# Performance work log

Hardware: AMD Instinct MI355X
Metric: run time of the kernel (lower is better)

The kernel has to match this reference:

```python
import jax, jax.numpy as jnp
import numpy as np

B, S, D, H, DFF = 2, 2048, 768, 12, 3072
DH = D // H
EPS = 1e-5


def _ln(x, g, b):
    m = jnp.mean(x, axis=-1, keepdims=True)
    v = jnp.mean((x - m) ** 2, axis=-1, keepdims=True)
    return (x - m) * jax.lax.rsqrt(v + EPS) * g + b


def setup_inputs() -> dict:
    key = jax.random.key(0)
    ks = jax.random.split(key, 13)
    sd = 1.0 / np.sqrt(D)
    sf = 1.0 / np.sqrt(DFF)
    return {
        "x": jax.random.normal(ks[0], (B, S, D), jnp.float32),
        "Wq": jax.random.uniform(ks[1], (D, D), jnp.float32, -sd, sd),
        "bq": jnp.zeros((D,), jnp.float32),
        "Wk": jax.random.uniform(ks[2], (D, D), jnp.float32, -sd, sd),
        "bk": jnp.zeros((D,), jnp.float32),
        "Wv": jax.random.uniform(ks[3], (D, D), jnp.float32, -sd, sd),
        "bv": jnp.zeros((D,), jnp.float32),
        "Wo": jax.random.uniform(ks[4], (D, D), jnp.float32, -sd, sd),
        "bo": jnp.zeros((D,), jnp.float32),
        "W1": jax.random.uniform(ks[5], (D, DFF), jnp.float32, -sd, sd),
        "b1": jnp.zeros((DFF,), jnp.float32),
        "W2": jax.random.uniform(ks[6], (DFF, D), jnp.float32, -sf, sf),
        "b2": jnp.zeros((D,), jnp.float32),
        "g1": jnp.ones((D,), jnp.float32),
        "be1": jnp.zeros((D,), jnp.float32),
        "g2": jnp.ones((D,), jnp.float32),
        "be2": jnp.zeros((D,), jnp.float32),
    }


def reference(x, Wq, bq, Wk, bk, Wv, bv, Wo, bo, W1, b1, W2, b2, g1, be1, g2, be2):
    # QKV projections, then split heads: [B,S,D] -> [B,H,S,DH]
    def heads(t):
        return t.reshape(B, S, H, DH).transpose(0, 2, 1, 3)
    Q = heads(x @ Wq + bq)
    K = heads(x @ Wk + bk)
    V = heads(x @ Wv + bv)
    # Per-head loop in original == batched-over-heads attention here (same math)
    scores = jnp.einsum("bhqd,bhkd->bhqk", Q, K) / np.sqrt(DH)
    attn = jax.nn.softmax(scores, axis=-1)  # [B,H,S,S] -- dominant intermediate
    ctx = jnp.einsum("bhqk,bhkd->bhqd", attn, V)
    ctx = ctx.transpose(0, 2, 1, 3).reshape(B, S, D)  # concat heads
    x = x + (ctx @ Wo + bo)
    x = _ln(x, g1, be1)
    ffn = (jax.nn.gelu(x @ W1 + b1, approximate=False)) @ W2 + b2
    x = _ln(x + ffn, g2, be2)
    return x
```

## Files before the change

### kernel.cpp

```cpp
#include <hip/hip_runtime.h>
#include <math.h>

#define BB 2
#define SS 2048
#define DD 768
#define HH 12
#define DHH 64
#define DFFN 3072
#define MTOK (BB*SS)

typedef __attribute__((ext_vector_type(8))) __bf16 bf16x8;
typedef __attribute__((ext_vector_type(4))) float f32x4;
typedef __attribute__((ext_vector_type(16))) float f32x16;

__device__ __forceinline__ unsigned short f2bf(float f) {
    unsigned int b = __builtin_bit_cast(unsigned int, f);
    b += 0x7FFFu + ((b >> 16) & 1u);
    return (unsigned short)(b >> 16);
}

__device__ __forceinline__ void gload_lds16(const void* g, void* l) {
    __builtin_amdgcn_global_load_lds((const __attribute__((address_space(1))) unsigned int*)g,
                                     (__attribute__((address_space(3))) unsigned int*)l,
                                     16, 0, 0);
}

template <int ACT, int OBF>
__global__ __launch_bounds__(256) void gemm_mfma(const unsigned short* __restrict__ A,
                                                 const unsigned short* __restrict__ Bt,
                                                 const float* __restrict__ bias,
                                                 void* __restrict__ Cout,
                                                 int M, int N, int ldA, int ldB, int Klen) {
    __shared__ unsigned short As[2 * 128 * 64];
    __shared__ unsigned short Bs[2 * 128 * 64];
    const int tid = threadIdx.x;
    const int lane = tid & 63;
    const int w = tid >> 6;
    const int l15 = lane & 15, l4 = lane >> 4;
    const int m0 = blockIdx.x * 128;
    const int n0 = blockIdx.y * 128;
    const int z = blockIdx.z;
    const int wr = (w >> 1) * 64;
    const int wc = (w & 1) * 64;

    const unsigned short* Az = A + (size_t)z * Klen;
    const unsigned short* Bz = Bt + (size_t)z * Klen;

    f32x4 acc[4][4] = {};

    int srow[4], scd[4];
#pragma unroll
    for (int i = 0; i < 4; ++i) {
        int s = w * 256 + i * 64 + lane;
        srow[i] = s >> 3;
        scd[i] = (((s & 7) ^ (srow[i] & 7))) * 8;
    }

#pragma unroll
    for (int i = 0; i < 4; ++i) {
        gload_lds16(Az + (size_t)(m0 + srow[i]) * ldA + scd[i], &As[(w * 256 + i * 64) * 8]);
        gload_lds16(Bz + (size_t)(n0 + srow[i]) * ldB + scd[i], &Bs[(w * 256 + i * 64) * 8]);
    }
    __syncthreads();

    int cb = 0;
    for (int k0 = 0; k0 < Klen; k0 += 64) {
        if (k0 + 64 < Klen) {
            const int nb = (cb ^ 1) * 128 * 64;
#pragma unroll
            for (int i = 0; i < 4; ++i) {
                gload_lds16(Az + (size_t)(m0 + srow[i]) * ldA + k0 + 64 + scd[i],
                            &As[nb + (w * 256 + i * 64) * 8]);
                gload_lds16(Bz + (size_t)(n0 + srow[i]) * ldB + k0 + 64 + scd[i],
                            &Bs[nb + (w * 256 + i * 64) * 8]);
            }
        }
        const unsigned short* Ac = &As[cb * 128 * 64];
        const unsigned short* Bc = &Bs[cb * 128 * 64];
#pragma unroll
        for (int ks = 0; ks < 2; ++ks) {
            bf16x8 af[4], bfr[4];
#pragma unroll
            for (int m = 0; m < 4; ++m) {
                int r = wr + m * 16 + l15;
                int c = (ks * 4 + l4) ^ (r & 7);
                af[m] = *(const bf16x8*)&Ac[(r * 8 + c) * 8];
            }
#pragma unroll
            for (int n = 0; n < 4; ++n) {
                int r = wc + n * 16 + l15;
                int c = (ks * 4 + l4) ^ (r & 7);
                bfr[n] = *(const bf16x8*)&Bc[(r * 8 + c) * 8];
            }
#pragma unroll
            for (int m = 0; m < 4; ++m)
#pragma unroll
                for (int n = 0; n < 4; ++n)
                    acc[m][n] = __builtin_amdgcn_mfma_f32_16x16x32_bf16(af[m], bfr[n], acc[m][n], 0, 0, 0);
        }
        __syncthreads();
        cb ^= 1;
    }

    const size_t zoff = (size_t)z * M * N;
#pragma unroll
    for (int n = 0; n < 4; ++n) {
        int col = n0 + wc + n * 16 + l15;
        float bv = bias ? bias[col] : 0.0f;
#pragma unroll
        for (int m = 0; m < 4; ++m) {
#pragma unroll
            for (int r = 0; r < 4; ++r) {
                int row = m0 + wr + m * 16 + l4 * 4 + r;
                float v = acc[m][n][r] + bv;
                if (ACT) v = 0.5f * v * (1.0f + erff(v * 0.70710678118654752f));
                if (OBF) ((unsigned short*)Cout)[(size_t)row * N + col] = f2bf(v);
                else     ((float*)Cout)[zoff + (size_t)row * N + col] = v;
            }
        }
    }
}

__global__ __launch_bounds__(256) void attn_mfma3(const unsigned short* __restrict__ QKV,
                                                  const unsigned short* __restrict__ Vt,
                                                  float* __restrict__ Opart,
                                                  float* __restrict__ ML) {
    __shared__ unsigned short Ks[2 * 64 * 64];
    __shared__ unsigned short Vs[2 * 64 * 64];
    const int tid = threadIdx.x;
    const int lane = tid & 63;
    const int w = tid >> 6;
    const int l31 = lane & 31;
    const int hi = lane >> 5;
    const int bh = blockIdx.y;
    const int b = bh / HH, h = bh % HH;
    const int z = blockIdx.z;
    const int q0 = blockIdx.x * 128 + w * 32;
    const float CLOG = 0.18033688011112042f;

    bf16x8 qf[4];
    {
        const unsigned short* qp = QKV + (size_t)(b * SS + q0 + l31) * 2304 + h * 64 + hi * 8;
        qf[0] = *(const bf16x8*)qp;
        qf[1] = *(const bf16x8*)(qp + 16);
        qf[2] = *(const bf16x8*)(qp + 32);
        qf[3] = *(const bf16x8*)(qp + 48);
    }

    f32x16 oacc[2] = {};
    float m_run = -1e30f, l_run = 0.0f;

    int arow[2], acd[2];
#pragma unroll
    for (int i = 0; i < 2; ++i) {
        int s = w * 128 + i * 64 + lane;
        arow[i] = s >> 3;
        acd[i] = ((s & 7) ^ (arow[i] & 7)) * 8;
    }

    const int kbase = z * (SS / 2);
#pragma unroll
    for (int i = 0; i < 2; ++i) {
        gload_lds16(QKV + (size_t)(b * SS + kbase + arow[i]) * 2304 + DD + h * 64 + acd[i],
                    &Ks[(w * 128 + i * 64) * 8]);
        gload_lds16(Vt + (size_t)(bh * 64 + arow[i]) * SS + kbase + acd[i],
                    &Vs[(w * 128 + i * 64) * 8]);
    }
    __syncthreads();

    int cb = 0;
    for (int it = 0; it < SS / 128; ++it) {
        if (it + 1 < SS / 128) {
            const int k0n = kbase + (it + 1) * 64;
            const int nb = (cb ^ 1) * 64 * 64;
#pragma unroll
            for (int i = 0; i < 2; ++i) {
                gload_lds16(QKV + (size_t)(b * SS + k0n + arow[i]) * 2304 + DD + h * 64 + acd[i],
                            &Ks[nb + (w * 128 + i * 64) * 8]);
                gload_lds16(Vt + (size_t)(bh * 64 + arow[i]) * SS + k0n + acd[i],
                            &Vs[nb + (w * 128 + i * 64) * 8]);
            }
        }
        const unsigned short* Kc = &Ks[cb * 64 * 64];
        const unsigned short* Vc = &Vs[cb * 64 * 64];

        f32x16 st[2] = {};
#pragma unroll
        for (int t = 0; t < 2; ++t) {
#pragma unroll
            for (int ks = 0; ks < 4; ++ks) {
                int row = 32 * t + l31;
                int ch = (2 * ks + hi) ^ (row & 7);
                bf16x8 kf = *(const bf16x8*)&Kc[(row * 8 + ch) * 8];
                st[t] = __builtin_amdgcn_mfma_f32_32x32x16_bf16(kf, qf[ks], st[t], 0, 0, 0);
            }
        }

        float pmax = st[0][0];
#pragma unroll
        for (int r = 1; r < 16; ++r) pmax = fmaxf(pmax, st[0][r]);
#pragma unroll
        for (int r = 0; r < 16; ++r) pmax = fmaxf(pmax, st[1][r]);
        pmax = fmaxf(pmax, __shfl_xor(pmax, 32));
        pmax *= CLOG;

        if (!__all(pmax <= m_run + 8.0f)) {
            float mn = fmaxf(m_run, pmax);
            float corr = exp2f(m_run - mn);
#pragma unroll
            for (int d = 0; d < 2; ++d)
#pragma unroll
                for (int r = 0; r < 16; ++r) oacc[d][r] *= corr;
            l_run *= corr;
            m_run = mn;
        }

        unsigned int Wn[2][4][2];
        float rs = 0.0f;
#pragma unroll
        for (int t = 0; t < 2; ++t) {
#pragma unroll
            for (int blk = 0; blk < 4; ++blk) {
                float pa = exp2f(fmaf(st[t][4 * blk + 0], CLOG, -m_run));
                float pb = exp2f(fmaf(st[t][4 * blk + 1], CLOG, -m_run));
                float pc = exp2f(fmaf(st[t][4 * blk + 2], CLOG, -m_run));
                float pd = exp2f(fmaf(st[t][4 * blk + 3], CLOG, -m_run));
                rs += (pa + pb) + (pc + pd);
                Wn[t][blk][0] = (unsigned int)f2bf(pa) | ((unsigned int)f2bf(pb) << 16);
                Wn[t][blk][1] = (unsigned int)f2bf(pc) | ((unsigned int)f2bf(pd) << 16);
            }
        }
        rs += __shfl_xor(rs, 32);
        l_run += rs;

#pragma unroll
        for (int t = 0; t < 2; ++t) {
#pragma unroll
            for (int ks2 = 0; ks2 < 2; ++ks2) {
                unsigned int ex0 = __shfl_xor(hi ? Wn[t][2 * ks2][0] : Wn[t][2 * ks2 + 1][0], 32);
                unsigned int ex1 = __shfl_xor(hi ? Wn[t][2 * ks2][1] : Wn[t][2 * ks2 + 1][1], 32);
                union { unsigned int u[4]; bf16x8 v; } pu;
                pu.u[0] = hi ? ex0 : Wn[t][2 * ks2][0];
                pu.u[1] = hi ? ex1 : Wn[t][2 * ks2][1];
                pu.u[2] = hi ? Wn[t][2 * ks2 + 1][0] : ex0;
                pu.u[3] = hi ? Wn[t][2 * ks2 + 1][1] : ex1;
#pragma unroll
                for (int d = 0; d < 2; ++d) {
                    int row = 32 * d + l31;
                    int ch = (4 * t + 2 * ks2 + hi) ^ (row & 7);
                    bf16x8 vf = *(const bf16x8*)&Vc[(row * 8 + ch) * 8];
                    oacc[d] = __builtin_amdgcn_mfma_f32_32x32x16_bf16(vf, pu.v, oacc[d], 0, 0, 0);
                }
            }
        }
        __syncthreads();
        cb ^= 1;
    }

    float* op = Opart + (size_t)z * MTOK * DD + (size_t)(b * SS + q0 + l31) * DD + h * 64;
#pragma unroll
    for (int d = 0; d < 2; ++d) {
#pragma unroll
        for (int blk = 0; blk < 4; ++blk) {
            float4 v = make_float4(oacc[d][4 * blk + 0], oacc[d][4 * blk + 1],
                                   oacc[d][4 * blk + 2], oacc[d][4 * blk + 3]);
            *(float4*)(op + 32 * d + 8 * blk + 4 * hi) = v;
        }
    }
    if (hi == 0) {
        size_t mi = (((size_t)z * BB * HH + bh) * SS + (q0 + l31)) * 2;
        ML[mi] = m_run;
        ML[mi + 1] = l_run;
    }
}

__global__ __launch_bounds__(256) void attn_combine(const float* __restrict__ Opart,
                                                    const float* __restrict__ ML,
                                                    unsigned short* __restrict__ Ctx) {
    const int row = blockIdx.x;
    const int tid = threadIdx.x;
    const int b = row >> 11, s = row & 2047;
    const float* r0 = Opart + (size_t)row * DD;
    const float* r1 = Opart + (size_t)MTOK * DD + (size_t)row * DD;
    unsigned short* co = Ctx + (size_t)row * DD;
#pragma unroll
    for (int i = 0; i < 3; ++i) {
        int c = tid + i * 256;
        int h = c >> 6;
        size_t i0 = (((size_t)(b * HH + h)) * SS + s) * 2;
        size_t i1 = (((size_t)(BB * HH + b * HH + h)) * SS + s) * 2;
        float m0 = ML[i0], l0 = ML[i0 + 1];
        float m1 = ML[i1], l1 = ML[i1 + 1];
        float M = fmaxf(m0, m1);
        float w0 = exp2f(m0 - M), w1 = exp2f(m1 - M);
        float inv = 1.0f / (w0 * l0 + w1 * l1);
        co[c] = f2bf((r0[c] * w0 + r1[c] * w1) * inv);
    }
}

__global__ __launch_bounds__(256) void v_transpose(const unsigned short* __restrict__ QKV,
                                                   unsigned short* __restrict__ Vt) {
    __shared__ unsigned short t[64][66];
    const int tid = threadIdx.x;
    const int bh = blockIdx.y, b = bh / HH, h = bh % HH;
    const int s0 = blockIdx.x * 64;
    const int c = tid & 63, r0 = tid >> 6;
#pragma unroll
    for (int i = 0; i < 16; ++i) {
        int r = i * 4 + r0;
        t[r][c] = QKV[(size_t)(b * SS + s0 + r) * 2304 + 1536 + h * 64 + c];
    }
    __syncthreads();
#pragma unroll
    for (int i = 0; i < 16; ++i) {
        int r = i * 4 + r0;
        Vt[((size_t)bh * 64 + r) * SS + s0 + c] = t[c][r];
    }
}

__global__ __launch_bounds__(256) void wtrans(const float* __restrict__ W,
                                              unsigned short* __restrict__ Wt,
                                              int K, int N, int rowoff) {
    __shared__ float t[32][33];
    const int tid = threadIdx.x;
    const int k0 = blockIdx.x * 32, n0 = blockIdx.y * 32;
    const int c = tid & 31, r0 = tid >> 5;
#pragma unroll
    for (int i = 0; i < 4; ++i) {
        int r = i * 8 + r0;
        t[r][c] = W[(size_t)(k0 + r) * N + n0 + c];
    }
    __syncthreads();
#pragma unroll
    for (int i = 0; i < 4; ++i) {
        int r = i * 8 + r0;
        Wt[(size_t)(rowoff + n0 + r) * K + k0 + c] = f2bf(t[c][r]);
    }
}

__global__ __launch_bounds__(256) void f2b_vec(const float* __restrict__ in,
                                               unsigned short* __restrict__ out, int n4) {
    int i = blockIdx.x * 256 + threadIdx.x;
    if (i < n4) {
        float4 v = ((const float4*)in)[i];
        unsigned long long pk = (unsigned long long)f2bf(v.x)
                              | ((unsigned long long)f2bf(v.y) << 16)
                              | ((unsigned long long)f2bf(v.z) << 32)
                              | ((unsigned long long)f2bf(v.w) << 48);
        ((unsigned long long*)out)[i] = pk;
    }
}

__global__ __launch_bounds__(256) void bias_concat(const float* __restrict__ q,
                                                   const float* __restrict__ k,
                                                   const float* __restrict__ v,
                                                   float* __restrict__ o) {
    int i = blockIdx.x * 256 + threadIdx.x;
    if (i < DD) { o[i] = q[i]; o[DD + i] = k[i]; o[2 * DD + i] = v[i]; }
}

template <int WB>
__global__ __launch_bounds__(256) void add_ln3(const float* __restrict__ a,
                                               const float* __restrict__ p1,
                                               const float* __restrict__ p2,
                                               const float* __restrict__ bias,
                                               const float* __restrict__ g,
                                               const float* __restrict__ be,
                                               float* __restrict__ outf,
                                               unsigned short* __restrict__ outb) {
    const int row = blockIdx.x;
    const int tid = threadIdx.x;
    float x[3];
    float s = 0.0f, s2 = 0.0f;
#pragma unroll
    for (int i = 0; i < 3; ++i) {
        int c = tid + i * 256;
        size_t idx = (size_t)row * DD + c;
        float v = a[idx] + p1[idx] + p2[idx] + bias[c];
        x[i] = v; s += v; s2 += v * v;
    }
#pragma unroll
    for (int off = 32; off; off >>= 1) {
        s += __shfl_down(s, off);
        s2 += __shfl_down(s2, off);
    }
    __shared__ float ws[8];
    const int wid = tid >> 6, lane = tid & 63;
    if (lane == 0) { ws[wid] = s; ws[4 + wid] = s2; }
    __syncthreads();
    if (tid == 0) {
        ws[0] = ws[0] + ws[1] + ws[2] + ws[3];
        ws[4] = ws[4] + ws[5] + ws[6] + ws[7];
    }
    __syncthreads();
    const float mean = ws[0] * (1.0f / DD);
    const float var = ws[4] * (1.0f / DD) - mean * mean;
    const float inv = rsqrtf(var + 1e-5f);
#pragma unroll
    for (int i = 0; i < 3; ++i) {
        int c = tid + i * 256;
        float res = (x[i] - mean) * inv * g[c] + be[c];
        outf[(size_t)row * DD + c] = res;
        if (WB) outb[(size_t)row * DD + c] = f2bf(res);
    }
}

extern "C" void kernel_launch(void* const* d_in, const int* in_sizes, int n_in,
                              void* d_out, int out_size, void* d_ws, size_t ws_size,
                              hipStream_t stream) {
    const float* x   = (const float*)d_in[0];
    const float* Wq  = (const float*)d_in[1];
    const float* bq  = (const float*)d_in[2];
    const float* Wk  = (const float*)d_in[3];
    const float* bk  = (const float*)d_in[4];
    const float* Wv  = (const float*)d_in[5];
    const float* bv  = (const float*)d_in[6];
    const float* Wo  = (const float*)d_in[7];
    const float* bo  = (const float*)d_in[8];
    const float* W1  = (const float*)d_in[9];
    const float* b1  = (const float*)d_in[10];
    const float* W2  = (const float*)d_in[11];
    const float* b2  = (const float*)d_in[12];
    const float* g1  = (const float*)d_in[13];
    const float* be1 = (const float*)d_in[14];
    const float* g2  = (const float*)d_in[15];
    const float* be2 = (const float*)d_in[16];
    float* out = (float*)d_out;

    char* w8 = (char*)d_ws;
    unsigned short* QKV = (unsigned short*)w8;
    unsigned short* Hff = (unsigned short*)w8;
    unsigned short* Vt  = (unsigned short*)(w8 + 18874368);
    unsigned short* Ctxb  = (unsigned short*)(w8 + 25165824);
    unsigned short* xb    = (unsigned short*)(w8 + 31457280);
    unsigned short* Wqkvt = (unsigned short*)(w8 + 37748736);
    unsigned short* Wot   = (unsigned short*)(w8 + 41287680);
    unsigned short* W1t   = (unsigned short*)(w8 + 42467328);
    unsigned short* W2t   = (unsigned short*)(w8 + 47185920);
    float* bqkv = (float*)(w8 + 51904512);
    float* Pa   = (float*)(w8 + 51916800);
    float* Pb   = (float*)(w8 + 64499712);
    float* X2   = (float*)(w8 + 77082624);
    float* ML   = (float*)(w8 + 89665536);

    dim3 blk(256);

    f2b_vec<<<dim3(3072), blk, 0, stream>>>(x, xb, MTOK * DD / 4);
    wtrans<<<dim3(24, 24), blk, 0, stream>>>(Wq, Wqkvt, DD, DD, 0);
    wtrans<<<dim3(24, 24), blk, 0, stream>>>(Wk, Wqkvt, DD, DD, DD);
    wtrans<<<dim3(24, 24), blk, 0, stream>>>(Wv, Wqkvt, DD, DD, 2 * DD);
    wtrans<<<dim3(24, 24), blk, 0, stream>>>(Wo, Wot, DD, DD, 0);
    wtrans<<<dim3(24, 96), blk, 0, stream>>>(W1, W1t, DD, DFFN, 0);
    wtrans<<<dim3(96, 24), blk, 0, stream>>>(W2, W2t, DFFN, DD, 0);
    bias_concat<<<dim3(3), blk, 0, stream>>>(bq, bk, bv, bqkv);

    gemm_mfma<0, 1><<<dim3(32, 18, 1), blk, 0, stream>>>(xb, Wqkvt, bqkv, QKV,
                                                         MTOK, 3 * DD, DD, DD, DD);
    v_transpose<<<dim3(32, 24), blk, 0, stream>>>(QKV, Vt);
    attn_mfma3<<<dim3(SS / 128, BB * HH, 2), blk, 0, stream>>>(QKV, Vt, Pa, ML);
    attn_combine<<<dim3(MTOK), blk, 0, stream>>>(Pa, ML, Ctxb);
    gemm_mfma<0, 0><<<dim3(32, 6, 2), blk, 0, stream>>>(Ctxb, Wot, nullptr, Pa,
                                                        MTOK, DD, DD, DD, 384);
    add_ln3<1><<<dim3(MTOK), blk, 0, stream>>>(x, Pa, Pb, bo, g1, be1, X2, xb);
    gemm_mfma<1, 1><<<dim3(32, 24, 1), blk, 0, stream>>>(xb, W1t, b1, Hff,
                                                         MTOK, DFFN, DD, DD, DD);
    gemm_mfma<0, 0><<<dim3(32, 6, 2), blk, 0, stream>>>(Hff, W2t, nullptr, Pa,
                                                        MTOK, DD, DFFN, DFFN, 1536);
    add_ln3<0><<<dim3(MTOK), blk, 0, stream>>>(X2, Pa, Pb, b2, g2, be2, out, nullptr);
}
```

Before: 345.7 us.

## Split attention KV range four ways, store bf16 partials, use permlane32 swap

Raises the split-KV factor of the flash-attention kernel from 2 to 4, so the grid has twice as many blocks and each processes a shorter key range. This targets low occupancy on the large GPU. Partial outputs are stored as bf16 instead of fp32 to keep the larger combine traffic in check, at some precision cost. Cross-half-wave reductions and the P fragment exchange now use permlane32_swap when it is available, in place of shuffle plus select. The combine kernel is generalised to merge an arbitrary number of splits.

```diff
diff --git a/kernel.cpp b/kernel.cpp
--- a/kernel.cpp
+++ b/kernel.cpp
@@ -8,6 +8,7 @@
 #define DHH 64
 #define DFFN 3072
 #define MTOK (BB*SS)
+#define KVSPL 4
 
 typedef __attribute__((ext_vector_type(8))) __bf16 bf16x8;
 typedef __attribute__((ext_vector_type(4))) float f32x4;
@@ -18,11 +19,47 @@
     b += 0x7FFFu + ((b >> 16) & 1u);
     return (unsigned short)(b >> 16);
 }
+__device__ __forceinline__ float bf2f(unsigned short u) {
+    unsigned int b = ((unsigned int)u) << 16;
+    return __builtin_bit_cast(float, b);
+}
 
 __device__ __forceinline__ void gload_lds16(const void* g, void* l) {
     __builtin_amdgcn_global_load_lds((const __attribute__((address_space(1))) unsigned int*)g,
                                      (__attribute__((address_space(3))) unsigned int*)l,
                                      16, 0, 0);
+}
+
+#if __has_builtin(__builtin_amdgcn_permlane32_swap)
+#define HAVE_PSWAP 1
+__device__ __forceinline__ void pswap(unsigned int x, unsigned int y,
+                                      unsigned int& r0, unsigned int& r1) {
+    auto r = __builtin_amdgcn_permlane32_swap(x, y, false, false);
+    r0 = r[0]; r1 = r[1];
+}
+#else
+#define HAVE_PSWAP 0
+__device__ __forceinline__ void pswap(unsigned int x, unsigned int y,
+                                      unsigned int& r0, unsigned int& r1) {
+    unsigned int xs = __shfl_xor(x, 32);
+    unsigned int ys = __shfl_xor(y, 32);
+    bool hi = (threadIdx.x & 32) != 0;
+    r0 = hi ? ys : x;
+    r1 = hi ? y : xs;
+}
+#endif
+
+__device__ __forceinline__ float xhalf_max(float v) {
+    unsigned int u = __builtin_bit_cast(unsigned int, v);
+    unsigned int a, b;
+    pswap(u, u, a, b);
+    return fmaxf(__builtin_bit_cast(float, a), __builtin_bit_cast(float, b));
+}
+__device__ __forceinline__ float xhalf_sum(float v) {
+    unsigned int u = __builtin_bit_cast(unsigned int, v);
+    unsigned int a, b;
+    pswap(u, u, a, b);
+    return __builtin_bit_cast(float, a) + __builtin_bit_cast(float, b);
 }
 
 template <int ACT, int OBF>
@@ -121,9 +158,9 @@
     }
 }
 
-__global__ __launch_bounds__(256) void attn_mfma3(const unsigned short* __restrict__ QKV,
+__global__ __launch_bounds__(256) void attn_mfma4(const unsigned short* __restrict__ QKV,
                                                   const unsigned short* __restrict__ Vt,
-                                                  float* __restrict__ Opart,
+                                                  unsigned short* __restrict__ Opart,
                                                   float* __restrict__ ML) {
     __shared__ unsigned short Ks[2 * 64 * 64];
     __shared__ unsigned short Vs[2 * 64 * 64];
@@ -158,7 +195,7 @@
         acd[i] = ((s & 7) ^ (arow[i] & 7)) * 8;
     }
 
-    const int kbase = z * (SS / 2);
+    const int kbase = z * (SS / KVSPL);
 #pragma unroll
     for (int i = 0; i < 2; ++i) {
         gload_lds16(QKV + (size_t)(b * SS + kbase + arow[i]) * 2304 + DD + h * 64 + acd[i],
@@ -169,8 +206,9 @@
     __syncthreads();
 
     int cb = 0;
-    for (int it = 0; it < SS / 128; ++it) {
-        if (it + 1 < SS / 128) {
+    const int NT = (SS / KVSPL) / 64;
+    for (int it = 0; it < NT; ++it) {
+        if (it + 1 < NT) {
             const int k0n = kbase + (it + 1) * 64;
             const int nb = (cb ^ 1) * 64 * 64;
 #pragma unroll
@@ -201,8 +239,7 @@
         for (int r = 1; r < 16; ++r) pmax = fmaxf(pmax, st[0][r]);
 #pragma unroll
         for (int r = 0; r < 16; ++r) pmax = fmaxf(pmax, st[1][r]);
-        pmax = fmaxf(pmax, __shfl_xor(pmax, 32));
-        pmax *= CLOG;
+        pmax = xhalf_max(pmax) * CLOG;
 
         if (!__all(pmax <= m_run + 8.0f)) {
             float mn = fmaxf(m_run, pmax);
@@ -230,20 +267,18 @@
                 Wn[t][blk][1] = (unsigned int)f2bf(pc) | ((unsigned int)f2bf(pd) << 16);
             }
         }
-        rs += __shfl_xor(rs, 32);
-        l_run += rs;
+        l_run += xhalf_sum(rs);
 
 #pragma unroll
         for (int t = 0; t < 2; ++t) {
 #pragma unroll
             for (int ks2 = 0; ks2 < 2; ++ks2) {
-                unsigned int ex0 = __shfl_xor(hi ? Wn[t][2 * ks2][0] : Wn[t][2 * ks2 + 1][0], 32);
-                unsigned int ex1 = __shfl_xor(hi ? Wn[t][2 * ks2][1] : Wn[t][2 * ks2 + 1][1], 32);
+                unsigned int a0, a1, b0, b1;
+                pswap(Wn[t][2 * ks2][0], Wn[t][2 * ks2 + 1][0], a0, a1);
+                pswap(Wn[t][2 * ks2][1], Wn[t][2 * ks2 + 1][1], b0, b1);
                 union { unsigned int u[4]; bf16x8 v; } pu;
-                pu.u[0] = hi ? ex0 : Wn[t][2 * ks2][0];
-                pu.u[1] = hi ? ex1 : Wn[t][2 * ks2][1];
-                pu.u[2] = hi ? Wn[t][2 * ks2 + 1][0] : ex0;
-                pu.u[3] = hi ? Wn[t][2 * ks2 + 1][1] : ex1;
+                pu.u[0] = a0; pu.u[1] = b0;
+                pu.u[2] = a1; pu.u[3] = b1;
 #pragma unroll
                 for (int d = 0; d < 2; ++d) {
                     int row = 32 * d + l31;
@@ -257,14 +292,17 @@
         cb ^= 1;
     }
 
-    float* op = Opart + (size_t)z * MTOK * DD + (size_t)(b * SS + q0 + l31) * DD + h * 64;
+    unsigned short* op = Opart + (size_t)z * MTOK * DD + (size_t)(b * SS + q0 + l31) * DD + h * 64;
 #pragma unroll
     for (int d = 0; d < 2; ++d) {
 #pragma unroll
         for (int blk = 0; blk < 4; ++blk) {
-            float4 v = make_float4(oacc[d][4 * blk + 0], oacc[d][4 * blk + 1],
-                                   oacc[d][4 * blk + 2], oacc[d][4 * blk + 3]);
-            *(float4*)(op + 32 * d + 8 * blk + 4 * hi) = v;
+            unsigned long long pk =
+                  (unsigned long long)f2bf(oacc[d][4 * blk + 0])
+                | ((unsigned long long)f2bf(oacc[d][4 * blk + 1]) << 16)
+                | ((unsigned long long)f2bf(oacc[d][4 * blk + 2]) << 32)
+                | ((unsigned long long)f2bf(oacc[d][4 * blk + 3]) << 48);
+            *(unsigned long long*)(op + 32 * d + 8 * blk + 4 * hi) = pk;
         }
     }
     if (hi == 0) {
@@ -274,27 +312,33 @@
     }
 }
 
-__global__ __launch_bounds__(256) void attn_combine(const float* __restrict__ Opart,
+__global__ __launch_bounds__(256) void attn_combine(const unsigned short* __restrict__ Opart,
                                                     const float* __restrict__ ML,
                                                     unsigned short* __restrict__ Ctx) {
     const int row = blockIdx.x;
     const int tid = threadIdx.x;
     const int b = row >> 11, s = row & 2047;
-    const float* r0 = Opart + (size_t)row * DD;
-    const float* r1 = Opart + (size_t)MTOK * DD + (size_t)row * DD;
     unsigned short* co = Ctx + (size_t)row * DD;
 #pragma unroll
     for (int i = 0; i < 3; ++i) {
         int c = tid + i * 256;
         int h = c >> 6;
-        size_t i0 = (((size_t)(b * HH + h)) * SS + s) * 2;
-        size_t i1 = (((size_t)(BB * HH + b * HH + h)) * SS + s) * 2;
-        float m0 = ML[i0], l0 = ML[i0 + 1];
-        float m1 = ML[i1], l1 = ML[i1 + 1];
-        float M = fmaxf(m0, m1);
-        float w0 = exp2f(m0 - M), w1 = exp2f(m1 - M);
-        float inv = 1.0f / (w0 * l0 + w1 * l1);
-        co[c] = f2bf((r0[c] * w0 + r1[c] * w1) * inv);
+        float m[KVSPL], l[KVSPL];
+        float M = -1e30f;
+#pragma unroll
+        for (int zz = 0; zz < KVSPL; ++zz) {
+            size_t mi = (((size_t)zz * BB * HH + b * HH + h) * SS + s) * 2;
+            m[zz] = ML[mi]; l[zz] = ML[mi + 1];
+            M = fmaxf(M, m[zz]);
+        }
+        float denom = 0.0f, num = 0.0f;
+#pragma unroll
+        for (int zz = 0; zz < KVSPL; ++zz) {
+            float wgt = exp2f(m[zz] - M);
+            denom += wgt * l[zz];
+            num += wgt * bf2f(Opart[(size_t)zz * MTOK * DD + (size_t)row * DD + c]);
+        }
+        co[c] = f2bf(num / denom);
     }
 }
 
@@ -438,6 +482,7 @@
     unsigned short* W1t   = (unsigned short*)(w8 + 42467328);
     unsigned short* W2t   = (unsigned short*)(w8 + 47185920);
     float* bqkv = (float*)(w8 + 51904512);
+    unsigned short* Ob = (unsigned short*)(w8 + 51916800);
     float* Pa   = (float*)(w8 + 51916800);
     float* Pb   = (float*)(w8 + 64499712);
     float* X2   = (float*)(w8 + 77082624);
@@ -457,8 +502,8 @@
     gemm_mfma<0, 1><<<dim3(32, 18, 1), blk, 0, stream>>>(xb, Wqkvt, bqkv, QKV,
                                                          MTOK, 3 * DD, DD, DD, DD);
     v_transpose<<<dim3(32, 24), blk, 0, stream>>>(QKV, Vt);
-    attn_mfma3<<<dim3(SS / 128, BB * HH, 2), blk, 0, stream>>>(QKV, Vt, Pa, ML);
-    attn_combine<<<dim3(MTOK), blk, 0, stream>>>(Pa, ML, Ctxb);
+    attn_mfma4<<<dim3(SS / 128, BB * HH, KVSPL), blk, 0, stream>>>(QKV, Vt, Ob, ML);
+    attn_combine<<<dim3(MTOK), blk, 0, stream>>>(Ob, ML, Ctxb);
     gemm_mfma<0, 0><<<dim3(32, 6, 2), blk, 0, stream>>>(Ctxb, Wot, nullptr, Pa,
                                                         MTOK, DD, DD, DD, 384);
     add_ln3<1><<<dim3(MTOK), blk, 0, stream>>>(x, Pa, Pb, bo, g1, be1, X2, xb);
```

Measured after the change: 345.2 us. Within noise of the previous version (-0.1%).
